# Performance work log

Hardware: AMD Instinct MI355X
Metric: run time of the kernel (lower is better)

The kernel has to match this reference:

```python
import jax, jax.numpy as jnp
import numpy as np

N = 4096        # num nodes == input_dim (required: [N,N] scores += [N,input_dim] dng)
D_IN = 4096
D_MODEL = 1024
K_W = 10        # num_weights
LN_EPS = 1e-5   # torch LayerNorm default


def setup_inputs() -> dict:
    key = jax.random.key(0)
    ks = jax.random.split(key, 16)
    s = 0.02  # small init so softmax over the [N,N] biased scores stays well-conditioned
    return {
        "x": jax.random.normal(ks[0], (N, D_IN), jnp.float32) * s,
        "adjacency_matrix": (jax.random.uniform(ks[1], (N, N)) < 0.01).astype(jnp.float32),
        "graph_metrics": jax.random.normal(ks[2], (N, N), jnp.float32) * s,
        "weights": jax.random.uniform(ks[3], (N, K_W), jnp.float32),
        "W_stack": jax.random.normal(ks[4], (K_W, D_IN, D_MODEL), jnp.float32) * s,
        "b_stack": jnp.zeros((K_W, D_MODEL), jnp.float32),
        "Wq": jax.random.normal(ks[5], (D_MODEL, D_MODEL), jnp.float32) * s,
        "bq": jnp.zeros((D_MODEL,), jnp.float32),
        "Wk": jax.random.normal(ks[6], (D_MODEL, D_MODEL), jnp.float32) * s,
        "bk": jnp.zeros((D_MODEL,), jnp.float32),
        "Wv": jax.random.normal(ks[7], (D_MODEL, D_MODEL), jnp.float32) * s,
        "bv": jnp.zeros((D_MODEL,), jnp.float32),
        "Wo": jax.random.normal(ks[8], (D_MODEL, D_IN), jnp.float32) * s,
        "bo": jnp.zeros((D_IN,), jnp.float32),
        "gamma": jnp.ones((D_MODEL,), jnp.float32),
        "beta": jnp.zeros((D_MODEL,), jnp.float32),
    }


def _layer_norm(h, gamma, beta):
    mu = jnp.mean(h, axis=-1, keepdims=True)
    var = jnp.mean(jnp.square(h - mu), axis=-1, keepdims=True)
    return (h - mu) * jax.lax.rsqrt(var + LN_EPS) * gamma + beta


def reference(x, adjacency_matrix, graph_metrics, weights,
              W_stack, b_stack, Wq, bq, Wk, bk, Wv, bv, Wo, bo, gamma, beta):
    A = adjacency_matrix  # [N,N] float
    # --- graph-derived additive bias (dng_scores) ---
    direct = A @ x                                   # [N, D_IN]
    inter = A @ A                                    # [N, N]
    row = jnp.sum(A, axis=1, keepdims=True)          # [N, 1]
    col = jnp.sum(A, axis=0, keepdims=True)          # [1, N]
    sim = inter / (row + col - inter + 1e-6)         # neighborhood similarity [N,N]
    dng = direct + sim @ x + graph_metrics @ x       # [N, D_IN] (== [N, N])
    # --- weighted input projection (apply_weights, vectorized over K_W linears) ---
    weighted_x = jnp.einsum('ni,kio,nk->no', x, W_stack, weights) + weights @ b_stack
    h = _layer_norm(weighted_x, gamma, beta)         # [N, D_MODEL]
    # --- single-head attention with additive dng bias ---
    Q = h @ Wq + bq
    K = h @ Wk + bk
    V = h @ Wv + bv
    scores = Q @ K.T / np.sqrt(D_MODEL).astype(np.float32) + dng  # [N, N]
    attn = jax.nn.softmax(scores, axis=-1)
    out = attn @ V                                   # [N, D_MODEL]
    y = out @ Wo + bo                                # [N, D_IN]; dropout is eval-mode identity
    return jax.nn.relu(y + dng)
```

## Files before the change

### kernel.cpp

```cpp
#include <hip/hip_runtime.h>
#include <hip/hip_bf16.h>

typedef unsigned short u16;
typedef __bf16 bf16x8 __attribute__((ext_vector_type(8)));
typedef float f32x4 __attribute__((ext_vector_type(4)));

__device__ __forceinline__ u16 f2bf(float v) {
    __hip_bfloat16 h = __float2bfloat16(v);
    return __builtin_bit_cast(u16, h);
}
__device__ __forceinline__ float bf2f(u16 v) {
    __hip_bfloat16 h = __builtin_bit_cast(__hip_bfloat16, v);
    return __bfloat162float(h);
}

__device__ __forceinline__ void gld_lds16(const u16* g, u16* l) {
    __builtin_amdgcn_global_load_lds(
        (const __attribute__((address_space(1))) unsigned int*)(const void*)g,
        (__attribute__((address_space(3))) unsigned int*)(void*)l, 16, 0, 0);
}


__global__ void k_convert_bf16(const float* __restrict__ s, u16* __restrict__ d, long n) {
    long i = ((long)blockIdx.x * 256 + threadIdx.x) * 4;
    if (i < n) {
        float4 v = *(const float4*)(s + i);
        u16 a = f2bf(v.x), b = f2bf(v.y), c = f2bf(v.z), e = f2bf(v.w);
        ushort4 o; o.x = a; o.y = b; o.z = c; o.w = e;
        *(ushort4*)(d + i) = o;
    }
}

__global__ void k_zero_f32(float* __restrict__ p) {
    float4 z; z.x = z.y = z.z = z.w = 0.f;
    ((float4*)p)[(size_t)blockIdx.x * 256 + threadIdx.x] = z;
}

__global__ void k_transpose_f32_bf16(const float* __restrict__ src, u16* __restrict__ dst,
                                     int R, int C, int ld_src, int ld_dst) {
    __shared__ u16 t[32][33];
    int c0 = blockIdx.x * 32, r0 = blockIdx.y * 32;
    int tx = threadIdx.x & 31, ty = threadIdx.x >> 5;
#pragma unroll
    for (int i = 0; i < 32; i += 8)
        t[ty + i][tx] = f2bf(src[(size_t)(r0 + ty + i) * ld_src + c0 + tx]);
    __syncthreads();
#pragma unroll
    for (int i = 0; i < 32; i += 8)
        dst[(size_t)(c0 + ty + i) * ld_dst + r0 + tx] = t[tx][ty + i];
}

__global__ void k_transpose_u16(const u16* __restrict__ src, u16* __restrict__ dst,
                                int R, int C, int ld_src, int ld_dst) {
    __shared__ u16 t[32][33];
    int c0 = blockIdx.x * 32, r0 = blockIdx.y * 32;
    int tx = threadIdx.x & 31, ty = threadIdx.x >> 5;
#pragma unroll
    for (int i = 0; i < 32; i += 8)
        t[ty + i][tx] = src[(size_t)(r0 + ty + i) * ld_src + c0 + tx];
    __syncthreads();
#pragma unroll
    for (int i = 0; i < 32; i += 8)
        dst[(size_t)(c0 + ty + i) * ld_dst + r0 + tx] = t[tx][ty + i];
}

__global__ void k_rowsum(const float* __restrict__ A, float* __restrict__ r) {
    __shared__ float sm[4];
    const float4* p = (const float4*)(A + (size_t)blockIdx.x * 4096);
    float s = 0.f;
#pragma unroll
    for (int j = 0; j < 4; ++j) {
        float4 v = p[threadIdx.x + j * 256];
        s += v.x + v.y + v.z + v.w;
    }
#pragma unroll
    for (int o = 32; o; o >>= 1) s += __shfl_down(s, o, 64);
    if ((threadIdx.x & 63) == 0) sm[threadIdx.x >> 6] = s;
    __syncthreads();
    if (threadIdx.x == 0) r[blockIdx.x] = sm[0] + sm[1] + sm[2] + sm[3];
}

__global__ void k_rowsum_bf16(const u16* __restrict__ A, float* __restrict__ r) {
    __shared__ float sm[4];
    const ushort4* p = (const ushort4*)(A + (size_t)blockIdx.x * 4096);
    float s = 0.f;
#pragma unroll
    for (int j = 0; j < 4; ++j) {
        ushort4 v = p[threadIdx.x + j * 256];
        s += bf2f(v.x) + bf2f(v.y) + bf2f(v.z) + bf2f(v.w);
    }
#pragma unroll
    for (int o = 32; o; o >>= 1) s += __shfl_down(s, o, 64);
    if ((threadIdx.x & 63) == 0) sm[threadIdx.x >> 6] = s;
    __syncthreads();
    if (threadIdx.x == 0) r[blockIdx.x] = sm[0] + sm[1] + sm[2] + sm[3];
}

__global__ void k_bias_concat(const float* __restrict__ bq, const float* __restrict__ bk,
                              const float* __restrict__ bv, float* __restrict__ o) {
    int i = blockIdx.x * 256 + threadIdx.x;
    o[i] = i < 1024 ? bq[i] : (i < 2048 ? bk[i - 1024] : bv[i - 2048]);
}

__global__ void k_layernorm(const float* __restrict__ wx, const float* __restrict__ gamma,
                            const float* __restrict__ beta, u16* __restrict__ h) {
    __shared__ float sm[8];
    size_t base = (size_t)blockIdx.x * 1024;
    float4 v = ((const float4*)(wx + base))[threadIdx.x];
    float s = v.x + v.y + v.z + v.w;
    float q = v.x * v.x + v.y * v.y + v.z * v.z + v.w * v.w;
#pragma unroll
    for (int o = 32; o; o >>= 1) { s += __shfl_down(s, o, 64); q += __shfl_down(q, o, 64); }
    int lane = threadIdx.x & 63, w = threadIdx.x >> 6;
    if (lane == 0) { sm[w] = s; sm[4 + w] = q; }
    __syncthreads();
    s = sm[0] + sm[1] + sm[2] + sm[3];
    q = sm[4] + sm[5] + sm[6] + sm[7];
    float mu = s * (1.f / 1024.f);
    float var = q * (1.f / 1024.f) - mu * mu;
    float rstd = rsqrtf(var + 1e-5f);
    int c = threadIdx.x * 4;
    ushort4 o;
    o.x = f2bf((v.x - mu) * rstd * gamma[c + 0] + beta[c + 0]);
    o.y = f2bf((v.y - mu) * rstd * gamma[c + 1] + beta[c + 1]);
    o.z = f2bf((v.z - mu) * rstd * gamma[c + 2] + beta[c + 2]);
    o.w = f2bf((v.w - mu) * rstd * gamma[c + 3] + beta[c + 3]);
    *(ushort4*)(h + base + c) = o;
}

__global__ void k_softmax(const float* __restrict__ S, u16* __restrict__ P) {
    __shared__ float sm[8];
    size_t base = (size_t)blockIdx.x * 4096;
    const float4* p = (const float4*)(S + base);
    float4 v[4];
#pragma unroll
    for (int j = 0; j < 4; ++j) v[j] = p[threadIdx.x + j * 256];
    float m = -3.4e38f;
#pragma unroll
    for (int j = 0; j < 4; ++j)
        m = fmaxf(m, fmaxf(fmaxf(v[j].x, v[j].y), fmaxf(v[j].z, v[j].w)));
#pragma unroll
    for (int o = 32; o; o >>= 1) m = fmaxf(m, __shfl_down(m, o, 64));
    int lane = threadIdx.x & 63, w = threadIdx.x >> 6;
    if (lane == 0) sm[w] = m;
    __syncthreads();
    m = fmaxf(fmaxf(sm[0], sm[1]), fmaxf(sm[2], sm[3]));
    float s = 0.f;
#pragma unroll
    for (int j = 0; j < 4; ++j) {
        v[j].x = __expf(v[j].x - m); v[j].y = __expf(v[j].y - m);
        v[j].z = __expf(v[j].z - m); v[j].w = __expf(v[j].w - m);
        s += v[j].x + v[j].y + v[j].z + v[j].w;
    }
#pragma unroll
    for (int o = 32; o; o >>= 1) s += __shfl_down(s, o, 64);
    if (lane == 0) sm[4 + w] = s;
    __syncthreads();
    s = sm[4] + sm[5] + sm[6] + sm[7];
    float inv = 1.f / s;
#pragma unroll
    for (int j = 0; j < 4; ++j) {
        ushort4 o;
        o.x = f2bf(v[j].x * inv); o.y = f2bf(v[j].y * inv);
        o.z = f2bf(v[j].z * inv); o.w = f2bf(v[j].w * inv);
        *(ushort4*)(P + base + (size_t)(threadIdx.x + j * 256) * 4) = o;
    }
}

#define EPI_M_BUILD 0
#define EPI_F32     1
#define EPI_WEIGHTED 2
#define EPI_QKV     3
#define EPI_SCORES  4
#define EPI_BF16    5
#define EPI_FINAL   6


template <int EPI>
__launch_bounds__(256, 2)
__global__ void gemm_bt(const u16* __restrict__ A, const u16* __restrict__ Bt,
                        int K, int lda, int ldb, int ldc,
                        void* __restrict__ Cout,
                        const float* __restrict__ e0, const float* __restrict__ e1,
                        const float* __restrict__ e2, const float* __restrict__ e3,
                        float scale, int kidx, size_t zb) {
    __shared__ __align__(16) u16 As[128 * 32];
    __shared__ __align__(16) u16 Bs[128 * 32];
    const int tid = threadIdx.x;
    const int m0 = blockIdx.y * 128, n0 = blockIdx.x * 128;
    const int lane = tid & 63, wave = tid >> 6;
    const int wm = (wave >> 1) * 64, wn = (wave & 1) * 64;
    const int fr = lane & 15, quad = lane >> 4;

    Bt += (size_t)blockIdx.z * zb;

    f32x4 acc[4][4] = {};

    const int ar = tid >> 2, ak = (tid & 3) * 8;
    const u16* gA0 = A + (size_t)(m0 + ar) * lda + ak;
    const u16* gA1 = gA0 + (size_t)64 * lda;
    const u16* gB0 = Bt + (size_t)(n0 + ar) * ldb + ak;
    const u16* gB1 = gB0 + (size_t)64 * ldb;
    u16* lA0 = As + tid * 8;
    u16* lA1 = As + (tid + 256) * 8;
    u16* lB0 = Bs + tid * 8;
    u16* lB1 = Bs + (tid + 256) * 8;

    for (int kk = 0; kk < K; kk += 32) {
        __syncthreads();
        gld_lds16(gA0 + kk, lA0);
        gld_lds16(gA1 + kk, lA1);
        gld_lds16(gB0 + kk, lB0);
        gld_lds16(gB1 + kk, lB1);
        __syncthreads();

        bf16x8 af[4], bfv[4];
#pragma unroll
        for (int i = 0; i < 4; ++i)
            af[i] = *(const bf16x8*)(As + (wm + i * 16 + fr) * 32 + quad * 8);
#pragma unroll
        for (int i = 0; i < 4; ++i)
            bfv[i] = *(const bf16x8*)(Bs + (wn + i * 16 + fr) * 32 + quad * 8);
#pragma unroll
        for (int mi = 0; mi < 4; ++mi)
#pragma unroll
            for (int ni = 0; ni < 4; ++ni)
                acc[mi][ni] = __builtin_amdgcn_mfma_f32_16x16x32_bf16(af[mi], bfv[ni], acc[mi][ni], 0, 0, 0);
    }

#pragma unroll
    for (int mi = 0; mi < 4; ++mi) {
#pragma unroll
        for (int r = 0; r < 4; ++r) {
            int row = m0 + wm + mi * 16 + quad * 4 + r;
#pragma unroll
            for (int ni = 0; ni < 4; ++ni) {
                int col = n0 + wn + ni * 16 + fr;
                float v = acc[mi][ni][r];
                size_t ci = (size_t)row * ldc + col;
                if constexpr (EPI == EPI_BF16) {
                    ((u16*)Cout)[ci] = f2bf(v);
                } else if constexpr (EPI == EPI_F32) {
                    ((float*)Cout)[ci] = v;
                }
            }
        }
    }
}


#define FENCE() asm volatile("" ::: "memory")
#define BAR8() { FENCE(); __builtin_amdgcn_s_barrier(); FENCE(); }

template <int EPI>
__launch_bounds__(512, 2)
__global__ void gemm8(const u16* __restrict__ Ag, const u16* __restrict__ Bt,
                      int K, int lda, int ldb, int ldc, void* __restrict__ Cout,
                      const float* __restrict__ e0, const float* __restrict__ e1,
                      const float* __restrict__ e2, const float* __restrict__ e3,
                      float scale) {
    __shared__ __align__(16) u16 S[65536];
    const int tid = threadIdx.x;
    const int bid = blockIdx.y * gridDim.x + blockIdx.x;
    const int nwg = gridDim.x * gridDim.y;
    const int swz = (bid & 7) * (nwg >> 3) + (bid >> 3);
    const int m0 = (swz / gridDim.x) * 256;
    const int n0 = (swz % gridDim.x) * 256;

    const int srow = tid >> 3;
    const int skc8 = ((tid & 7) ^ (srow & 7)) * 8;
    const u16* gA = Ag + (size_t)(m0 + srow) * lda + skc8;
    const u16* gB = Bt + (size_t)(n0 + srow) * ldb + skc8;
    u16* dst = S + tid * 8;

    const int lane = tid & 63, wave = tid >> 6;
    const int wn = (wave & 3) * 64;
    const int wmA = (wave >> 2) * 64;
    const int fr = lane & 15, quad = lane >> 4;
    const int kc0 = (quad ^ (fr & 7)) * 8;
    const int kc1 = ((quad ^ (fr & 7)) ^ 4) * 8;

#define ISSUE_A(b, s, kk) { \
    gld_lds16(gA + (size_t)((s) * 64) * lda + (kk), dst + (b) * 32768 + (s) * 8192); \
    gld_lds16(gA + (size_t)((s) * 64 + 128) * lda + (kk), dst + (b) * 32768 + (s) * 8192 + 4096); }
#define ISSUE_B(b, s, kk) { \
    gld_lds16(gB + (size_t)((s) * 128) * ldb + (kk), dst + (b) * 32768 + 16384 + (s) * 8192); \
    gld_lds16(gB + (size_t)((s) * 128 + 64) * ldb + (kk), dst + (b) * 32768 + 16384 + (s) * 8192 + 4096); }

    ISSUE_A(0, 0, 0); ISSUE_B(0, 0, 0); ISSUE_B(0, 1, 0); ISSUE_A(0, 1, 0);
    ISSUE_A(1, 0, 64); ISSUE_B(1, 0, 64); ISSUE_B(1, 1, 64);

    f32x4 acc[8][4] = {};
    const int NT = K >> 6;

#define AR8(q, f, ks) (*(const bf16x8*)(SA + (((q) >> 1) * 128 + wmA + ((q) & 1) * 32 + (f) * 16 + fr) * 64 + ((ks) ? kc1 : kc0)))
#define PHASE(q) { \
    bf16x8 a00 = AR8(q, 0, 0), a01 = AR8(q, 0, 1), a10 = AR8(q, 1, 0), a11 = AR8(q, 1, 1); \
    __builtin_amdgcn_s_setprio(1); \
    _Pragma("unroll") \
    for (int fn = 0; fn < 4; ++fn) { \
        acc[2 * (q)][fn]     = __builtin_amdgcn_mfma_f32_16x16x32_bf16(a00, bfr[fn][0], acc[2 * (q)][fn], 0, 0, 0); \
        acc[2 * (q) + 1][fn] = __builtin_amdgcn_mfma_f32_16x16x32_bf16(a10, bfr[fn][0], acc[2 * (q) + 1][fn], 0, 0, 0); \
    } \
    _Pragma("unroll") \
    for (int fn = 0; fn < 4; ++fn) { \
        acc[2 * (q)][fn]     = __builtin_amdgcn_mfma_f32_16x16x32_bf16(a01, bfr[fn][1], acc[2 * (q)][fn], 0, 0, 0); \
        acc[2 * (q) + 1][fn] = __builtin_amdgcn_mfma_f32_16x16x32_bf16(a11, bfr[fn][1], acc[2 * (q) + 1][fn], 0, 0, 0); \
    } \
    __builtin_amdgcn_s_setprio(0); \
    asm volatile("s_waitcnt lgkmcnt(0)" ::: "memory"); }

    for (int t = 0; t < NT; ++t) {
        const int b = t & 1;
        const u16* SA = S + b * 32768;
        const u16* SB = SA + 16384;
        if (t + 1 < NT) ISSUE_A(b ^ 1, 1, (t + 1) * 64);
        if (t < NT - 1) { asm volatile("s_waitcnt vmcnt(8)" ::: "memory"); }
        else            { asm volatile("s_waitcnt vmcnt(0)" ::: "memory"); }
        BAR8();
        bf16x8 bfr[4][2];
#pragma unroll
        for (int fn = 0; fn < 4; ++fn) {
            bfr[fn][0] = *(const bf16x8*)(SB + (wn + fn * 16 + fr) * 64 + kc0);
            bfr[fn][1] = *(const bf16x8*)(SB + (wn + fn * 16 + fr) * 64 + kc1);
        }
        PHASE(0);
        BAR8();
        PHASE(1);
        BAR8();
        if (t + 2 < NT) ISSUE_A(b, 0, (t + 2) * 64);
        PHASE(2);
        BAR8();
        if (t + 2 < NT) { ISSUE_B(b, 0, (t + 2) * 64); ISSUE_B(b, 1, (t + 2) * 64); }
        PHASE(3);
        BAR8();
    }

    const int wmC = (wave >> 2) * 128;
#pragma unroll
    for (int fm = 0; fm < 8; ++fm) {
#pragma unroll
        for (int r = 0; r < 4; ++r) {
            const int row = m0 + wmC + fm * 16 + quad * 4 + r;
#pragma unroll
            for (int fn = 0; fn < 4; ++fn) {
                const int col = n0 + wn + fn * 16 + fr;
                float vv = acc[fm][fn][r];
                if constexpr (EPI == EPI_M_BUILD) {
                    size_t gi = (size_t)row * 4096 + col;
                    float denom = e2[row] + e3[col] - vv + 1e-6f;
                    ((u16*)Cout)[gi] = f2bf(e0[gi] + vv / denom + e1[gi]);
                } else if constexpr (EPI == EPI_F32) {
                    ((float*)Cout)[(size_t)row * ldc + col] = vv;
                } else if constexpr (EPI == EPI_WEIGHTED) {
                    atomicAdd((float*)Cout + (size_t)row * 1024 + (col & 1023),
                              e0[(size_t)row * 10 + (col >> 10)] * (vv + e1[col]));
                } else if constexpr (EPI == EPI_QKV) {
                    ((u16*)Cout)[(size_t)row * ldc + col] = f2bf(vv + e0[col]);
                } else if constexpr (EPI == EPI_SCORES) {
                    ((float*)Cout)[(size_t)row * ldc + col] = vv * scale + e0[(size_t)row * 4096 + col];
                } else {
                    float y = vv + e0[col] + e1[(size_t)row * 4096 + col];
                    ((float*)Cout)[(size_t)row * ldc + col] = y > 0.f ? y : 0.f;
                }
            }
        }
    }
#undef ISSUE_A
#undef ISSUE_B
#undef AR8
#undef PHASE
}


extern "C" void kernel_launch(void* const* d_in, const int* in_sizes, int n_in,
                              void* d_out, int out_size, void* d_ws, size_t ws_size,
                              hipStream_t stream) {
    (void)in_sizes; (void)n_in; (void)out_size; (void)ws_size;
    const float* x   = (const float*)d_in[0];
    const float* A   = (const float*)d_in[1];
    const float* gm  = (const float*)d_in[2];
    const float* wts = (const float*)d_in[3];
    const float* Wst = (const float*)d_in[4];
    const float* bst = (const float*)d_in[5];
    const float* Wq  = (const float*)d_in[6];
    const float* bq  = (const float*)d_in[7];
    const float* Wk  = (const float*)d_in[8];
    const float* bk  = (const float*)d_in[9];
    const float* Wv  = (const float*)d_in[10];
    const float* bv  = (const float*)d_in[11];
    const float* Wo  = (const float*)d_in[12];
    const float* bo  = (const float*)d_in[13];
    const float* gamma = (const float*)d_in[14];
    const float* beta  = (const float*)d_in[15];
    float* out = (float*)d_out;
    char* ws = (char*)d_ws;

    const int N = 4096, DM = 1024;
    const size_t MB32 = 33554432UL;
    u16*   A_bf   = (u16*)(ws + 0);
    u16*   A_bfT  = (u16*)(ws + MB32);
    float* scores = (float*)(ws + 0);
    u16*   x_bfT  = (u16*)(ws + 2 * MB32);
    u16*   attn   = (u16*)(ws + 2 * MB32);
    u16*   x_bf   = (u16*)(ws + 3 * MB32);
    u16*   WqkvT  = (u16*)(ws + 3 * MB32);
    float* bqkv   = (float*)(ws + 3 * MB32 + 6291456UL);
    u16*   QKV    = (u16*)(ws + 3 * MB32 + 6307840UL);
    u16*   M_bf   = (u16*)(ws + 4 * MB32);
    u16*   WallT  = (u16*)(ws + 0);
    u16*   V_T    = (u16*)(ws + 4 * MB32);
    u16*   WoT    = (u16*)(ws + 4 * MB32 + 8388608UL);
    u16*   out_bf = (u16*)(ws + 4 * MB32 + 16777216UL);
    float* dng    = (float*)(ws + 5 * MB32);
    float* wxf    = (float*)(ws + 5 * MB32 + 67108864UL);
    u16*   h_bf   = (u16*)(ws + 5 * MB32 + 83886080UL);
    float* rowS   = (float*)(ws + 5 * MB32 + 92274688UL);
    float* colS   = (float*)(ws + 5 * MB32 + 92291072UL);

    k_convert_bf16<<<16384, 256, 0, stream>>>(A, A_bf, (long)N * N);
    k_transpose_f32_bf16<<<dim3(128, 128), 256, 0, stream>>>(A, A_bfT, N, N, N, N);
    k_convert_bf16<<<16384, 256, 0, stream>>>(x, x_bf, (long)N * N);
    k_transpose_f32_bf16<<<dim3(128, 128), 256, 0, stream>>>(x, x_bfT, N, N, N, N);
    k_rowsum<<<N, 256, 0, stream>>>(A, rowS);
    k_rowsum_bf16<<<N, 256, 0, stream>>>(A_bfT, colS);

    gemm8<EPI_M_BUILD><<<dim3(16, 16), 512, 0, stream>>>(
        A_bf, A_bfT, N, N, N, N, M_bf, A, gm, rowS, colS, 0.f);

    gemm8<EPI_F32><<<dim3(16, 16), 512, 0, stream>>>(
        M_bf, x_bfT, N, N, N, N, dng, nullptr, nullptr, nullptr, nullptr, 0.f);

    for (int k = 0; k < 10; ++k)
        k_transpose_f32_bf16<<<dim3(32, 128), 256, 0, stream>>>(
            Wst + (size_t)k * N * DM, WallT + (size_t)k * DM * N, N, DM, DM, N);
    k_zero_f32<<<4096, 256, 0, stream>>>(wxf);
    gemm8<EPI_WEIGHTED><<<dim3(40, 16), 512, 0, stream>>>(
        x_bf, WallT, N, N, N, DM, wxf, wts, bst, nullptr, nullptr, 0.f);

    k_transpose_f32_bf16<<<dim3(32, 32), 256, 0, stream>>>(Wq, WqkvT, DM, DM, DM, DM);
    k_transpose_f32_bf16<<<dim3(32, 32), 256, 0, stream>>>(Wk, WqkvT + (size_t)DM * DM, DM, DM, DM, DM);
    k_transpose_f32_bf16<<<dim3(32, 32), 256, 0, stream>>>(Wv, WqkvT + 2 * (size_t)DM * DM, DM, DM, DM, DM);
    k_bias_concat<<<12, 256, 0, stream>>>(bq, bk, bv, bqkv);
    k_layernorm<<<N, 256, 0, stream>>>(wxf, gamma, beta, h_bf);

    gemm8<EPI_QKV><<<dim3(12, 16), 512, 0, stream>>>(
        h_bf, WqkvT, DM, DM, DM, 3072, QKV, bqkv, nullptr, nullptr, nullptr, 0.f);

    k_transpose_u16<<<dim3(32, 128), 256, 0, stream>>>(QKV + 2048, V_T, N, DM, 3072, N);

    gemm8<EPI_SCORES><<<dim3(16, 16), 512, 0, stream>>>(
        QKV, QKV + 1024, DM, 3072, 3072, N, scores, dng, nullptr, nullptr, nullptr, 0.03125f);

    k_softmax<<<N, 256, 0, stream>>>(scores, attn);

    gemm_bt<EPI_BF16><<<dim3(8, 32), 256, 0, stream>>>(
        attn, V_T, N, N, N, DM, out_bf, nullptr, nullptr, nullptr, nullptr, 0.f, 0, 0);

    k_transpose_f32_bf16<<<dim3(128, 32), 256, 0, stream>>>(Wo, WoT, DM, N, N, DM);
    gemm8<EPI_FINAL><<<dim3(16, 16), 512, 0, stream>>>(
        out_bf, WoT, DM, DM, DM, N, out, bo, dng, nullptr, nullptr, 0.f);
}
```

Baseline: 1.392 ms.

## Restructure gemm8 main loop to overlap LDS reads with barriers and loads

Splits each phase of the 256x256 bf16 GEMM loop into separate LDS-read and MFMA steps. Fragment reads and global-to-LDS issues now happen before a barrier, followed by an lgkmcnt wait and a sched_barrier, so LDS latency overlaps the barrier wait. The order of the global-load issues and the vmcnt thresholds change to match, and the prologue now waits before entering the loop. The goal is to hide LDS and global latency across phases, at the cost of more barriers per iteration and tighter buffer-reuse ordering that could race if the counts are wrong.

After: 1.400 ms. Within noise of the previous version (+0.5%).

```diff
diff --git a/kernel.cpp b/kernel.cpp
--- a/kernel.cpp
+++ b/kernel.cpp
@@ -251,6 +251,7 @@
 
 #define FENCE() asm volatile("" ::: "memory")
 #define BAR8() { FENCE(); __builtin_amdgcn_s_barrier(); FENCE(); }
+#define LGKM0() { asm volatile("s_waitcnt lgkmcnt(0)" ::: "memory"); __builtin_amdgcn_sched_barrier(0); }
 
 template <int EPI>
 __launch_bounds__(512, 2)
@@ -287,15 +288,27 @@
     gld_lds16(gB + (size_t)((s) * 128) * ldb + (kk), dst + (b) * 32768 + 16384 + (s) * 8192); \
     gld_lds16(gB + (size_t)((s) * 128 + 64) * ldb + (kk), dst + (b) * 32768 + 16384 + (s) * 8192 + 4096); }
 
-    ISSUE_A(0, 0, 0); ISSUE_B(0, 0, 0); ISSUE_B(0, 1, 0); ISSUE_A(0, 1, 0);
-    ISSUE_A(1, 0, 64); ISSUE_B(1, 0, 64); ISSUE_B(1, 1, 64);
-
     f32x4 acc[8][4] = {};
     const int NT = K >> 6;
 
+    ISSUE_A(0, 0, 0); ISSUE_A(0, 1, 0); ISSUE_B(0, 0, 0); ISSUE_B(0, 1, 0);
+    if (NT > 1) {
+        ISSUE_B(1, 0, 64); ISSUE_B(1, 1, 64); ISSUE_A(1, 0, 64);
+        asm volatile("s_waitcnt vmcnt(6)" ::: "memory");
+    } else {
+        asm volatile("s_waitcnt vmcnt(0)" ::: "memory");
+    }
+    BAR8();
+
 #define AR8(q, f, ks) (*(const bf16x8*)(SA + (((q) >> 1) * 128 + wmA + ((q) & 1) * 32 + (f) * 16 + fr) * 64 + ((ks) ? kc1 : kc0)))
-#define PHASE(q) { \
-    bf16x8 a00 = AR8(q, 0, 0), a01 = AR8(q, 0, 1), a10 = AR8(q, 1, 0), a11 = AR8(q, 1, 1); \
+#define READ_B() { \
+    _Pragma("unroll") \
+    for (int fn = 0; fn < 4; ++fn) { \
+        bfr[fn][0] = *(const bf16x8*)(SB + (wn + fn * 16 + fr) * 64 + kc0); \
+        bfr[fn][1] = *(const bf16x8*)(SB + (wn + fn * 16 + fr) * 64 + kc1); \
+    } }
+#define READ_A(q) { a00 = AR8(q, 0, 0); a01 = AR8(q, 0, 1); a10 = AR8(q, 1, 0); a11 = AR8(q, 1, 1); }
+#define MFMA_Q(q) { \
     __builtin_amdgcn_s_setprio(1); \
     _Pragma("unroll") \
     for (int fn = 0; fn < 4; ++fn) { \
@@ -307,32 +320,34 @@
         acc[2 * (q)][fn]     = __builtin_amdgcn_mfma_f32_16x16x32_bf16(a01, bfr[fn][1], acc[2 * (q)][fn], 0, 0, 0); \
         acc[2 * (q) + 1][fn] = __builtin_amdgcn_mfma_f32_16x16x32_bf16(a11, bfr[fn][1], acc[2 * (q) + 1][fn], 0, 0, 0); \
     } \
-    __builtin_amdgcn_s_setprio(0); \
-    asm volatile("s_waitcnt lgkmcnt(0)" ::: "memory"); }
+    __builtin_amdgcn_s_setprio(0); }
 
     for (int t = 0; t < NT; ++t) {
         const int b = t & 1;
         const u16* SA = S + b * 32768;
         const u16* SB = SA + 16384;
+        bf16x8 bfr[4][2], a00, a01, a10, a11;
+        READ_B(); READ_A(0);
         if (t + 1 < NT) ISSUE_A(b ^ 1, 1, (t + 1) * 64);
-        if (t < NT - 1) { asm volatile("s_waitcnt vmcnt(8)" ::: "memory"); }
+        BAR8(); LGKM0();
+        MFMA_Q(0);
+        BAR8();
+        READ_A(1);
+        if (t + 2 < NT) ISSUE_B(b, 0, (t + 2) * 64);
+        BAR8(); LGKM0();
+        MFMA_Q(1);
+        BAR8();
+        READ_A(2);
+        if (t + 2 < NT) ISSUE_B(b, 1, (t + 2) * 64);
+        BAR8(); LGKM0();
+        MFMA_Q(2);
+        BAR8();
+        READ_A(3);
+        if (t + 2 < NT) ISSUE_A(b, 0, (t + 2) * 64);
+        if (t < NT - 2) { asm volatile("s_waitcnt vmcnt(6)" ::: "memory"); }
         else            { asm volatile("s_waitcnt vmcnt(0)" ::: "memory"); }
-        BAR8();
-        bf16x8 bfr[4][2];
-#pragma unroll
-        for (int fn = 0; fn < 4; ++fn) {
-            bfr[fn][0] = *(const bf16x8*)(SB + (wn + fn * 16 + fr) * 64 + kc0);
-            bfr[fn][1] = *(const bf16x8*)(SB + (wn + fn * 16 + fr) * 64 + kc1);
-        }
-        PHASE(0);
-        BAR8();
-        PHASE(1);
-        BAR8();
-        if (t + 2 < NT) ISSUE_A(b, 0, (t + 2) * 64);
-        PHASE(2);
-        BAR8();
-        if (t + 2 < NT) { ISSUE_B(b, 0, (t + 2) * 64); ISSUE_B(b, 1, (t + 2) * 64); }
-        PHASE(3);
+        BAR8(); LGKM0();
+        MFMA_Q(3);
         BAR8();
     }
 
@@ -369,7 +384,9 @@
 #undef ISSUE_A
 #undef ISSUE_B
 #undef AR8
-#undef PHASE
+#undef READ_B
+#undef READ_A
+#undef MFMA_Q
 }
 
 
```
